# Optimization experiments

Measured on AMD Instinct MI355X. Metric: run time of the kernel, lower is better.

The kernel has to match this reference:

```python
import jax, jax.numpy as jnp
import numpy as np

def setup_inputs() -> dict:
    key = jax.random.key(0)
    ks = jax.random.split(key, 8)
    B, C, H, W = 4, 64, 64, 64
    Cr = C // 8
    s = 1.0 / np.sqrt(C)
    return {
        "x": jax.random.normal(ks[0], (B, C, H, W), jnp.float32),
        "wq": jax.random.normal(ks[1], (Cr, C), jnp.float32) * s,
        "bq": jax.random.normal(ks[2], (Cr,), jnp.float32) * 0.01,
        "wk": jax.random.normal(ks[3], (Cr, C), jnp.float32) * s,
        "bk": jax.random.normal(ks[4], (Cr,), jnp.float32) * 0.01,
        "wv": jax.random.normal(ks[5], (C, C), jnp.float32) * s,
        "bv": jax.random.normal(ks[6], (C,), jnp.float32) * 0.01,
        "gamma": jax.random.normal(ks[7], (1,), jnp.float32) * 0.1,
    }

def reference(x, wq, bq, wk, bk, wv, bv, gamma):
    B, C, H, W = x.shape
    N = H * W
    xf = x.reshape(B, C, N)  # 1x1 conv == pointwise linear over channel dim
    q = jnp.einsum("oc,bcn->bno", wq, xf) + bq[None, None, :]   # (B, N, Cr)
    k = jnp.einsum("oc,bcn->bon", wk, xf) + bk[None, :, None]   # (B, Cr, N)
    v = jnp.einsum("oc,bcn->bon", wv, xf) + bv[None, :, None]   # (B, C, N)
    attn = jnp.einsum("bno,bom->bnm", q, k)                     # (B, N, N)
    attn = jax.nn.softmax(attn, axis=-1)
    out = jnp.einsum("bcm,bnm->bcn", v, attn)                   # (B, C, N)
    out = out.reshape(B, C, H, W)
    return x + gamma[0] * out
```

## Files before the change

kernel.cpp:

```cpp
#include <hip/hip_runtime.h>

#define BB 4
#define CC 64
#define NN 4096

typedef __attribute__((ext_vector_type(8)))  short short8;
typedef __attribute__((ext_vector_type(4)))  short short4v;
typedef __attribute__((ext_vector_type(4)))  float f32x4;
typedef __attribute__((ext_vector_type(16))) float f32x16;
typedef unsigned short u16;

#define QWS_ELEMS (BB * NN * 8)

__device__ inline u16 f2bf(float x) {
    unsigned u = __float_as_uint(x);
    u = (u + 0x7fffu + ((u >> 16) & 1u)) >> 16;
    return (u16)u;
}
__device__ inline unsigned pack2rne(float a, float b) {
    return (unsigned)f2bf(a) | ((unsigned)f2bf(b) << 16);
}
__device__ inline unsigned permpack(float lo, float hi) {
    return __builtin_amdgcn_perm(__float_as_uint(hi), __float_as_uint(lo), 0x07060302);
}

__device__ inline void barrier_lgkm() {
    asm volatile("s_waitcnt lgkmcnt(0)\n\ts_barrier" ::: "memory");
}

union SH8 {
    short8 s;
    struct Halves { short4v lo, hi; } h;
    uint4 u;
};

__global__ __launch_bounds__(512) void proj_kernel(
    const float* __restrict__ x,
    const float* __restrict__ wq, const float* __restrict__ bq,
    const float* __restrict__ wk, const float* __restrict__ bk,
    const float* __restrict__ wv, const float* __restrict__ bv,
    u16* __restrict__ ws_u)
{
    u16* qws = ws_u;
    u16* kws = ws_u + QWS_ELEMS;
    u16* vws = ws_u + 2 * QWS_ELEMS;

    const int y   = blockIdx.y;
    const int pix = blockIdx.x * 512 + threadIdx.x;
    const int b   = pix >> 12;
    const int n   = pix & (NN - 1);
    const float* xb = x + ((size_t)b << 18) + n;

    if (y < 8) {
        const int v0 = y << 3;
        float av[8];
#pragma unroll
        for (int i = 0; i < 8; ++i) av[i] = bv[v0 + i];
#pragma unroll 8
        for (int c = 0; c < CC; ++c) {
            const float xv = xb[(size_t)c << 12];
#pragma unroll
            for (int i = 0; i < 8; ++i)
                av[i] += wv[(v0 + i) * CC + c] * xv;
        }
#pragma unroll
        for (int i = 0; i < 8; ++i)
            vws[(((size_t)((b << 6) + v0 + i)) << 12) + n] = f2bf(av[i]);
    } else {
        float aq[8], ak[8];
#pragma unroll
        for (int i = 0; i < 8; ++i) { aq[i] = bq[i]; ak[i] = bk[i]; }
#pragma unroll 8
        for (int c = 0; c < CC; ++c) {
            const float xv = xb[(size_t)c << 12];
#pragma unroll
            for (int i = 0; i < 8; ++i) {
                aq[i] += wq[i * CC + c] * xv;
                ak[i] += wk[i * CC + c] * xv;
            }
        }
        uint4 qp, kp;
        qp.x = pack2rne(aq[0], aq[1]); qp.y = pack2rne(aq[2], aq[3]);
        qp.z = pack2rne(aq[4], aq[5]); qp.w = pack2rne(aq[6], aq[7]);
        kp.x = pack2rne(ak[0], ak[1]); kp.y = pack2rne(ak[2], ak[3]);
        kp.z = pack2rne(ak[4], ak[5]); kp.w = pack2rne(ak[6], ak[7]);
        *(uint4*)&qws[(size_t)pix * 8] = qp;
        *(uint4*)&kws[(size_t)pix * 8] = kp;
    }
}

__global__ __launch_bounds__(512) void attn_kernel(
    const float* __restrict__ x, const float* __restrict__ gamma,
    const u16* __restrict__ ws_u, float* __restrict__ out)
{
    const u16* qws = ws_u;
    const u16* kws = ws_u + QWS_ELEMS;
    const u16* vws = ws_u + 2 * QWS_ELEMS;

    __shared__ __align__(16) char smem[34816 + 1024 + 256];
    u16*   v_t    = (u16*)smem;
    float* eb     = (float*)smem;
    float* l_part = (float*)(smem + 34816);
    float* l_inv  = (float*)(smem + 34816 + 1024);

    const int tid  = threadIdx.x;
    const int w    = tid >> 6;
    const int lane = tid & 63;
    const int l31  = lane & 31;
    const int lh   = lane >> 5;
    const int mh   = w >> 1;
    const int qh   = w & 1;

    const int b  = blockIdx.y;
    const int qb = blockIdx.x << 6;
    const int bN = b << 12;

    short8 qf = {0,0,0,0,0,0,0,0};
    short8 kf = {0,0,0,0,0,0,0,0};
    if (lane < 32) {
        qf = *(const short8*)(qws + (size_t)(bN + qb + (qh << 5) + l31) * 8);
        kf = *(const short8*)(kws + (size_t)(bN + (mh << 5) + l31) * 8);
    }
    short8 kn = kf;

    const int c_st = tid >> 3;
    const int o_st = (tid & 7) << 3;
    const u16* vgr = vws + (((size_t)((b << 6) + c_st)) << 12) + o_st;
    const int st0  = c_st * 132 + o_st;

    SH8 va0, va1, vb0, vb1;
    va0.s = *(const short8*)(vgr);
    va1.s = *(const short8*)(vgr + 64);
    *(short4v*)&v_t[st0]      = va0.h.lo;
    *(short4v*)&v_t[st0 + 4]  = va0.h.hi;
    *(short4v*)&v_t[st0 + 64] = va1.h.lo;
    *(short4v*)&v_t[st0 + 68] = va1.h.hi;
    va0.s = *(const short8*)(vgr + 128);
    va1.s = *(const short8*)(vgr + 192);

    const int rA = l31 * 132;
    const int rB = (32 + l31) * 132;
    const int mb = (mh << 5) + (lh << 2);

    f32x16 z16, acc0, acc1;
#pragma unroll
    for (int r = 0; r < 16; ++r) { z16[r] = 0.f; acc0[r] = 0.f; acc1[r] = 0.f; }
    float ls = 0.f;

    barrier_lgkm();

#pragma unroll 2
    for (int it = 0; it < 32; ++it) {
        const int buf = (it & 1) * (CC * 132);
        const int nxt = ((it + 1) & 31) << 7;
        const int nx2 = ((it + 2) & 31) << 7;

        vb0.s = *(const short8*)(vgr + nx2);
        vb1.s = *(const short8*)(vgr + nx2 + 64);
        if (lane < 32)
            kn = *(const short8*)(kws + (size_t)(bN + nxt + (mh << 5) + l31) * 8);

        f32x16 d = __builtin_amdgcn_mfma_f32_32x32x16_bf16(kf, qf, z16, 0, 0, 0);

        float p[16];
#pragma unroll
        for (int r = 0; r < 16; ++r) p[r] = __expf(d[r]);
        float s0 = 0.f, s1 = 0.f;
#pragma unroll
        for (int r = 0; r < 8; ++r) { s0 += p[2 * r]; s1 += p[2 * r + 1]; }
        ls += s0 + s1;

        SH8 A0, A1;
        A0.u.x = permpack(p[0],  p[1]);  A0.u.y = permpack(p[2],  p[3]);
        A0.u.z = permpack(p[4],  p[5]);  A0.u.w = permpack(p[6],  p[7]);
        A1.u.x = permpack(p[8],  p[9]);  A1.u.y = permpack(p[10], p[11]);
        A1.u.z = permpack(p[12], p[13]); A1.u.w = permpack(p[14], p[15]);

        SH8 B00, B01, B10, B11;
        B00.h.lo = *(const short4v*)&v_t[buf + rA + mb];
        B00.h.hi = *(const short4v*)&v_t[buf + rA + mb + 8];
        B01.h.lo = *(const short4v*)&v_t[buf + rB + mb];
        B01.h.hi = *(const short4v*)&v_t[buf + rB + mb + 8];
        B10.h.lo = *(const short4v*)&v_t[buf + rA + mb + 16];
        B10.h.hi = *(const short4v*)&v_t[buf + rA + mb + 24];
        B11.h.lo = *(const short4v*)&v_t[buf + rB + mb + 16];
        B11.h.hi = *(const short4v*)&v_t[buf + rB + mb + 24];

        acc0 = __builtin_amdgcn_mfma_f32_32x32x16_bf16(A0.s, B00.s, acc0, 0, 0, 0);
        acc1 = __builtin_amdgcn_mfma_f32_32x32x16_bf16(A0.s, B01.s, acc1, 0, 0, 0);
        acc0 = __builtin_amdgcn_mfma_f32_32x32x16_bf16(A1.s, B10.s, acc0, 0, 0, 0);
        acc1 = __builtin_amdgcn_mfma_f32_32x32x16_bf16(A1.s, B11.s, acc1, 0, 0, 0);

        const int ob = (CC * 132) - buf;
        *(short4v*)&v_t[ob + st0]      = va0.h.lo;
        *(short4v*)&v_t[ob + st0 + 4]  = va0.h.hi;
        *(short4v*)&v_t[ob + st0 + 64] = va1.h.lo;
        *(short4v*)&v_t[ob + st0 + 68] = va1.h.hi;
        va0 = vb0; va1 = vb1;
        kf = kn;

        barrier_lgkm();
    }

    float lt = ls + __shfl_xor(ls, 32, 64);
    if (lane < 32) l_part[(mh * 2 + qh) * 32 + l31] = lt;
    __syncthreads();
    if (w < 2 && lane < 32) {
        float s = l_part[(0 * 2 + qh) * 32 + l31] + l_part[(1 * 2 + qh) * 32 + l31]
                + l_part[(2 * 2 + qh) * 32 + l31] + l_part[(3 * 2 + qh) * 32 + l31];
        l_inv[qh * 32 + l31] = 1.0f / s;
    }

    if (mh >= 2) {
        float* e0 = &eb[(((mh - 2) << 2) + (qh << 1) + 0) * 1088 + lane * 17];
        float* e1 = &eb[(((mh - 2) << 2) + (qh << 1) + 1) * 1088 + lane * 17];
#pragma unroll
        for (int r = 0; r < 16; ++r) { e0[r] = acc0[r]; e1[r] = acc1[r]; }
    }
    __syncthreads();
    if (mh < 2) {
        const float* e0 = &eb[((mh << 2) + (qh << 1) + 0) * 1088 + lane * 17];
        const float* e1 = &eb[((mh << 2) + (qh << 1) + 1) * 1088 + lane * 17];
#pragma unroll
        for (int r = 0; r < 16; ++r) { acc0[r] += e0[r]; acc1[r] += e1[r]; }
    }
    __syncthreads();
    if (mh == 1) {
        float* e0 = &eb[((qh << 1) + 0) * 1088 + lane * 17];
        float* e1 = &eb[((qh << 1) + 1) * 1088 + lane * 17];
#pragma unroll
        for (int r = 0; r < 16; ++r) { e0[r] = acc0[r]; e1[r] = acc1[r]; }
    }
    __syncthreads();
    if (w < 2) {
        const float* e0 = &eb[((qh << 1) + 0) * 1088 + lane * 17];
        const float* e1 = &eb[((qh << 1) + 1) * 1088 + lane * 17];
#pragma unroll
        for (int r = 0; r < 16; ++r) { acc0[r] += e0[r]; acc1[r] += e1[r]; }

        f32x4 li[4];
#pragma unroll
        for (int k = 0; k < 4; ++k)
            li[k] = *(const f32x4*)&l_inv[qh * 32 + (k << 3) + (lh << 2)];
        const float g = gamma[0];
#pragma unroll
        for (int ch = 0; ch < 2; ++ch) {
            const int c = (ch << 5) + l31;
            const f32x16 a = ch ? acc1 : acc0;
            const size_t rowb = (((size_t)((b << 6) + c)) << 12) + qb + (qh << 5);
#pragma unroll
            for (int k = 0; k < 4; ++k) {
                const int q0 = (k << 3) + (lh << 2);
                const float4 xv = *(const float4*)&x[rowb + q0];
                float4 o;
                o.x = xv.x + g * a[4 * k + 0] * li[k][0];
                o.y = xv.y + g * a[4 * k + 1] * li[k][1];
                o.z = xv.z + g * a[4 * k + 2] * li[k][2];
                o.w = xv.w + g * a[4 * k + 3] * li[k][3];
                *(float4*)&out[rowb + q0] = o;
            }
        }
    }
}

extern "C" void kernel_launch(void* const* d_in, const int* in_sizes, int n_in,
                              void* d_out, int out_size, void* d_ws, size_t ws_size,
                              hipStream_t stream)
{
    const float* x     = (const float*)d_in[0];
    const float* wq    = (const float*)d_in[1];
    const float* bq    = (const float*)d_in[2];
    const float* wk    = (const float*)d_in[3];
    const float* bk    = (const float*)d_in[4];
    const float* wv    = (const float*)d_in[5];
    const float* bv    = (const float*)d_in[6];
    const float* gamma = (const float*)d_in[7];
    u16*   ws  = (u16*)d_ws;
    float* out = (float*)d_out;

    hipLaunchKernelGGL(proj_kernel, dim3(BB * NN / 512, 9), dim3(512), 0, stream,
                       x, wq, bq, wk, bk, wv, bv, ws);
    hipLaunchKernelGGL(attn_kernel, dim3(NN / 64, BB), dim3(512), 0, stream,
                       x, gamma, ws, out);
}
```

Baseline: 105.9 us.

## Shrink attention blocks to 32 queries and 4 waves, doubling grid size

Each attention block now handles 32 query rows with 4 waves that split the key dimension, instead of 64 query rows with 8 waves. The grid doubles to 512 blocks so the GPU's compute units have more blocks to schedule and balance. The V staging loads are reorganized so 256 threads fill the same 64x128 tile. The cost is that each block re-streams the full K and V for only half as many queries, doubling global and LDS traffic per unit of work. The 2x loop unroll is also dropped.

```diff
diff --git a/kernel.cpp b/kernel.cpp
--- a/kernel.cpp
+++ b/kernel.cpp
@@ -89,7 +89,7 @@
     }
 }
 
-__global__ __launch_bounds__(512) void attn_kernel(
+__global__ __launch_bounds__(256) void attn_kernel(
     const float* __restrict__ x, const float* __restrict__ gamma,
     const u16* __restrict__ ws_u, float* __restrict__ out)
 {
@@ -97,50 +97,49 @@
     const u16* kws = ws_u + QWS_ELEMS;
     const u16* vws = ws_u + 2 * QWS_ELEMS;
 
-    __shared__ __align__(16) char smem[34816 + 1024 + 256];
+    __shared__ __align__(16) char smem[33792 + 512 + 128];
     u16*   v_t    = (u16*)smem;
     float* eb     = (float*)smem;
-    float* l_part = (float*)(smem + 34816);
-    float* l_inv  = (float*)(smem + 34816 + 1024);
+    float* l_part = (float*)(smem + 33792);
+    float* l_inv  = (float*)(smem + 33792 + 512);
 
     const int tid  = threadIdx.x;
     const int w    = tid >> 6;
     const int lane = tid & 63;
     const int l31  = lane & 31;
     const int lh   = lane >> 5;
-    const int mh   = w >> 1;
-    const int qh   = w & 1;
 
     const int b  = blockIdx.y;
-    const int qb = blockIdx.x << 6;
+    const int qb = blockIdx.x << 5;
     const int bN = b << 12;
 
     short8 qf = {0,0,0,0,0,0,0,0};
     short8 kf = {0,0,0,0,0,0,0,0};
     if (lane < 32) {
-        qf = *(const short8*)(qws + (size_t)(bN + qb + (qh << 5) + l31) * 8);
-        kf = *(const short8*)(kws + (size_t)(bN + (mh << 5) + l31) * 8);
+        qf = *(const short8*)(qws + (size_t)(bN + qb + l31) * 8);
+        kf = *(const short8*)(kws + (size_t)(bN + (w << 5) + l31) * 8);
     }
     short8 kn = kf;
 
-    const int c_st = tid >> 3;
-    const int o_st = (tid & 7) << 3;
-    const u16* vgr = vws + (((size_t)((b << 6) + c_st)) << 12) + o_st;
-    const int st0  = c_st * 132 + o_st;
-
-    SH8 va0, va1, vb0, vb1;
-    va0.s = *(const short8*)(vgr);
-    va1.s = *(const short8*)(vgr + 64);
-    *(short4v*)&v_t[st0]      = va0.h.lo;
-    *(short4v*)&v_t[st0 + 4]  = va0.h.hi;
-    *(short4v*)&v_t[st0 + 64] = va1.h.lo;
-    *(short4v*)&v_t[st0 + 68] = va1.h.hi;
-    va0.s = *(const short8*)(vgr + 128);
-    va1.s = *(const short8*)(vgr + 192);
+    const int c_st = tid >> 2;
+    const int oq   = (tid & 3) << 3;
+    const u16* vgr = vws + (((size_t)((b << 6) + c_st)) << 12) + oq;
+    const int st0  = c_st * 132 + oq;
+
+    SH8 va[4], vb[4];
+#pragma unroll
+    for (int j = 0; j < 4; ++j) {
+        va[j].s = *(const short8*)(vgr + 32 * j);
+        *(short4v*)&v_t[st0 + 32 * j]     = va[j].h.lo;
+        *(short4v*)&v_t[st0 + 32 * j + 4] = va[j].h.hi;
+    }
+#pragma unroll
+    for (int j = 0; j < 4; ++j)
+        va[j].s = *(const short8*)(vgr + 128 + 32 * j);
 
     const int rA = l31 * 132;
     const int rB = (32 + l31) * 132;
-    const int mb = (mh << 5) + (lh << 2);
+    const int mb = (w << 5) + (lh << 2);
 
     f32x16 z16, acc0, acc1;
 #pragma unroll
@@ -149,16 +148,16 @@
 
     barrier_lgkm();
 
-#pragma unroll 2
     for (int it = 0; it < 32; ++it) {
-        const int buf = (it & 1) * (CC * 132);
+        const int buf = (it & 1) * 8448;
         const int nxt = ((it + 1) & 31) << 7;
         const int nx2 = ((it + 2) & 31) << 7;
 
-        vb0.s = *(const short8*)(vgr + nx2);
-        vb1.s = *(const short8*)(vgr + nx2 + 64);
+#pragma unroll
+        for (int j = 0; j < 4; ++j)
+            vb[j].s = *(const short8*)(vgr + nx2 + 32 * j);
         if (lane < 32)
-            kn = *(const short8*)(kws + (size_t)(bN + nxt + (mh << 5) + l31) * 8);
+            kn = *(const short8*)(kws + (size_t)(bN + nxt + (w << 5) + l31) * 8);
 
         f32x16 d = __builtin_amdgcn_mfma_f32_32x32x16_bf16(kf, qf, z16, 0, 0, 0);
 
@@ -191,63 +190,63 @@
         acc0 = __builtin_amdgcn_mfma_f32_32x32x16_bf16(A1.s, B10.s, acc0, 0, 0, 0);
         acc1 = __builtin_amdgcn_mfma_f32_32x32x16_bf16(A1.s, B11.s, acc1, 0, 0, 0);
 
-        const int ob = (CC * 132) - buf;
-        *(short4v*)&v_t[ob + st0]      = va0.h.lo;
-        *(short4v*)&v_t[ob + st0 + 4]  = va0.h.hi;
-        *(short4v*)&v_t[ob + st0 + 64] = va1.h.lo;
-        *(short4v*)&v_t[ob + st0 + 68] = va1.h.hi;
-        va0 = vb0; va1 = vb1;
+        const int ob = 8448 - buf;
+#pragma unroll
+        for (int j = 0; j < 4; ++j) {
+            *(short4v*)&v_t[ob + st0 + 32 * j]     = va[j].h.lo;
+            *(short4v*)&v_t[ob + st0 + 32 * j + 4] = va[j].h.hi;
+        }
+#pragma unroll
+        for (int j = 0; j < 4; ++j) va[j] = vb[j];
         kf = kn;
 
         barrier_lgkm();
     }
 
     float lt = ls + __shfl_xor(ls, 32, 64);
-    if (lane < 32) l_part[(mh * 2 + qh) * 32 + l31] = lt;
-    __syncthreads();
-    if (w < 2 && lane < 32) {
-        float s = l_part[(0 * 2 + qh) * 32 + l31] + l_part[(1 * 2 + qh) * 32 + l31]
-                + l_part[(2 * 2 + qh) * 32 + l31] + l_part[(3 * 2 + qh) * 32 + l31];
-        l_inv[qh * 32 + l31] = 1.0f / s;
-    }
-
-    if (mh >= 2) {
-        float* e0 = &eb[(((mh - 2) << 2) + (qh << 1) + 0) * 1088 + lane * 17];
-        float* e1 = &eb[(((mh - 2) << 2) + (qh << 1) + 1) * 1088 + lane * 17];
+    if (lane < 32) l_part[(w << 5) + l31] = lt;
+    __syncthreads();
+    if (w == 0 && lane < 32)
+        l_inv[l31] = 1.0f / (l_part[l31] + l_part[32 + l31] +
+                             l_part[64 + l31] + l_part[96 + l31]);
+
+    if (w >= 2) {
+        float* e0 = &eb[(((w - 2) << 1) + 0) * 1088 + lane * 17];
+        float* e1 = &eb[(((w - 2) << 1) + 1) * 1088 + lane * 17];
 #pragma unroll
         for (int r = 0; r < 16; ++r) { e0[r] = acc0[r]; e1[r] = acc1[r]; }
     }
     __syncthreads();
-    if (mh < 2) {
-        const float* e0 = &eb[((mh << 2) + (qh << 1) + 0) * 1088 + lane * 17];
-        const float* e1 = &eb[((mh << 2) + (qh << 1) + 1) * 1088 + lane * 17];
+    if (w < 2) {
+        const float* e0 = &eb[((w << 1) + 0) * 1088 + lane * 17];
+        const float* e1 = &eb[((w << 1) + 1) * 1088 + lane * 17];
 #pragma unroll
         for (int r = 0; r < 16; ++r) { acc0[r] += e0[r]; acc1[r] += e1[r]; }
     }
     __syncthreads();
-    if (mh == 1) {
-        float* e0 = &eb[((qh << 1) + 0) * 1088 + lane * 17];
-        float* e1 = &eb[((qh << 1) + 1) * 1088 + lane * 17];
+    if (w == 1) {
+        float* e0 = &eb[0 * 1088 + lane * 17];
+        float* e1 = &eb[1 * 1088 + lane * 17];
 #pragma unroll
         for (int r = 0; r < 16; ++r) { e0[r] = acc0[r]; e1[r] = acc1[r]; }
     }
     __syncthreads();
-    if (w < 2) {
-        const float* e0 = &eb[((qh << 1) + 0) * 1088 + lane * 17];
-        const float* e1 = &eb[((qh << 1) + 1) * 1088 + lane * 17];
+    if (w == 0) {
+        const float* e0 = &eb[0 * 1088 + lane * 17];
+        const float* e1 = &eb[1 * 1088 + lane * 17];
 #pragma unroll
         for (int r = 0; r < 16; ++r) { acc0[r] += e0[r]; acc1[r] += e1[r]; }
 
         f32x4 li[4];
 #pragma unroll
         for (int k = 0; k < 4; ++k)
-            li[k] = *(const f32x4*)&l_inv[qh * 32 + (k << 3) + (lh << 2)];
+            li[k] = *(const f32x4*)&l_inv[(k << 3) + (lh << 2)];
         const float g = gamma[0];
 #pragma unroll
         for (int ch = 0; ch < 2; ++ch) {
             const int c = (ch << 5) + l31;
             const f32x16 a = ch ? acc1 : acc0;
-            const size_t rowb = (((size_t)((b << 6) + c)) << 12) + qb + (qh << 5);
+            const size_t rowb = (((size_t)((b << 6) + c)) << 12) + qb;
 #pragma unroll
             for (int k = 0; k < 4; ++k) {
                 const int q0 = (k << 3) + (lh << 2);
@@ -280,6 +279,6 @@
 
     hipLaunchKernelGGL(proj_kernel, dim3(BB * NN / 512, 9), dim3(512), 0, stream,
                        x, wq, bq, wk, bk, wv, bv, ws);
-    hipLaunchKernelGGL(attn_kernel, dim3(NN / 64, BB), dim3(512), 0, stream,
+    hipLaunchKernelGGL(attn_kernel, dim3(NN / 32, BB), dim3(256), 0, stream,
                        x, gamma, ws, out);
 }
```

After: 111.5 us. 5.3% more time.

## Fuse projection and attention into one cooperative kernel with grid sync

Applied to the files above, without the earlier changes.

Merges the projection and attention kernels into a single cooperative launch of 256 blocks. A grid-wide sync separates the two phases. The projection phase is re-split so each block computes 10 output channels for 512 pixels. Q is pre-scaled by log2(e) so the softmax can use exp2f instead of __expf. This removes one kernel launch and its gap, at the cost of a grid barrier, scattered 2-byte q/k stores, and needing all 256 blocks to be co-resident.

```diff
diff --git a/kernel.cpp b/kernel.cpp
--- a/kernel.cpp
+++ b/kernel.cpp
@@ -1,8 +1,12 @@
 #include <hip/hip_runtime.h>
+#include <hip/hip_cooperative_groups.h>
+
+namespace cg = cooperative_groups;
 
 #define BB 4
 #define CC 64
 #define NN 4096
+#define LOG2E 1.44269504088896340736f
 
 typedef __attribute__((ext_vector_type(8)))  short short8;
 typedef __attribute__((ext_vector_type(4)))  short short4v;
@@ -17,9 +21,6 @@
     u = (u + 0x7fffu + ((u >> 16) & 1u)) >> 16;
     return (u16)u;
 }
-__device__ inline unsigned pack2rne(float a, float b) {
-    return (unsigned)f2bf(a) | ((unsigned)f2bf(b) << 16);
-}
 __device__ inline unsigned permpack(float lo, float hi) {
     return __builtin_amdgcn_perm(__float_as_uint(hi), __float_as_uint(lo), 0x07060302);
 }
@@ -34,68 +35,17 @@
     uint4 u;
 };
 
-__global__ __launch_bounds__(512) void proj_kernel(
+__global__ __launch_bounds__(512) void fused_kernel(
     const float* __restrict__ x,
     const float* __restrict__ wq, const float* __restrict__ bq,
     const float* __restrict__ wk, const float* __restrict__ bk,
     const float* __restrict__ wv, const float* __restrict__ bv,
-    u16* __restrict__ ws_u)
+    const float* __restrict__ gamma,
+    u16* __restrict__ ws_u, float* __restrict__ out)
 {
     u16* qws = ws_u;
     u16* kws = ws_u + QWS_ELEMS;
     u16* vws = ws_u + 2 * QWS_ELEMS;
-
-    const int y   = blockIdx.y;
-    const int pix = blockIdx.x * 512 + threadIdx.x;
-    const int b   = pix >> 12;
-    const int n   = pix & (NN - 1);
-    const float* xb = x + ((size_t)b << 18) + n;
-
-    if (y < 8) {
-        const int v0 = y << 3;
-        float av[8];
-#pragma unroll
-        for (int i = 0; i < 8; ++i) av[i] = bv[v0 + i];
-#pragma unroll 8
-        for (int c = 0; c < CC; ++c) {
-            const float xv = xb[(size_t)c << 12];
-#pragma unroll
-            for (int i = 0; i < 8; ++i)
-                av[i] += wv[(v0 + i) * CC + c] * xv;
-        }
-#pragma unroll
-        for (int i = 0; i < 8; ++i)
-            vws[(((size_t)((b << 6) + v0 + i)) << 12) + n] = f2bf(av[i]);
-    } else {
-        float aq[8], ak[8];
-#pragma unroll
-        for (int i = 0; i < 8; ++i) { aq[i] = bq[i]; ak[i] = bk[i]; }
-#pragma unroll 8
-        for (int c = 0; c < CC; ++c) {
-            const float xv = xb[(size_t)c << 12];
-#pragma unroll
-            for (int i = 0; i < 8; ++i) {
-                aq[i] += wq[i * CC + c] * xv;
-                ak[i] += wk[i * CC + c] * xv;
-            }
-        }
-        uint4 qp, kp;
-        qp.x = pack2rne(aq[0], aq[1]); qp.y = pack2rne(aq[2], aq[3]);
-        qp.z = pack2rne(aq[4], aq[5]); qp.w = pack2rne(aq[6], aq[7]);
-        kp.x = pack2rne(ak[0], ak[1]); kp.y = pack2rne(ak[2], ak[3]);
-        kp.z = pack2rne(ak[4], ak[5]); kp.w = pack2rne(ak[6], ak[7]);
-        *(uint4*)&qws[(size_t)pix * 8] = qp;
-        *(uint4*)&kws[(size_t)pix * 8] = kp;
-    }
-}
-
-__global__ __launch_bounds__(512) void attn_kernel(
-    const float* __restrict__ x, const float* __restrict__ gamma,
-    const u16* __restrict__ ws_u, float* __restrict__ out)
-{
-    const u16* qws = ws_u;
-    const u16* kws = ws_u + QWS_ELEMS;
-    const u16* vws = ws_u + 2 * QWS_ELEMS;
 
     __shared__ __align__(16) char smem[34816 + 1024 + 256];
     u16*   v_t    = (u16*)smem;
@@ -103,161 +53,205 @@
     float* l_part = (float*)(smem + 34816);
     float* l_inv  = (float*)(smem + 34816 + 1024);
 
-    const int tid  = threadIdx.x;
-    const int w    = tid >> 6;
-    const int lane = tid & 63;
-    const int l31  = lane & 31;
-    const int lh   = lane >> 5;
-    const int mh   = w >> 1;
-    const int qh   = w & 1;
-
-    const int b  = blockIdx.y;
-    const int qb = blockIdx.x << 6;
-    const int bN = b << 12;
-
-    short8 qf = {0,0,0,0,0,0,0,0};
-    short8 kf = {0,0,0,0,0,0,0,0};
-    if (lane < 32) {
-        qf = *(const short8*)(qws + (size_t)(bN + qb + (qh << 5) + l31) * 8);
-        kf = *(const short8*)(kws + (size_t)(bN + (mh << 5) + l31) * 8);
+    const int tid = threadIdx.x;
+    const int blk = blockIdx.x;
+
+    {
+        const int pg  = blk & 31;
+        const int sl  = blk >> 5;
+        const int o0  = sl * 10;
+        const int pix = (pg << 9) + tid;
+        const int b   = pix >> 12;
+        const int n   = pix & (NN - 1);
+        const float* xb = x + ((size_t)b << 18) + n;
+
+        const float* wrow[10];
+        float acc[10];
+#pragma unroll
+        for (int i = 0; i < 10; ++i) {
+            const int o = o0 + i;
+            if (o < 8)       { wrow[i] = wq + o * CC;        acc[i] = bq[o]; }
+            else if (o < 16) { wrow[i] = wk + (o - 8) * CC;  acc[i] = bk[o - 8]; }
+            else             { wrow[i] = wv + (o - 16) * CC; acc[i] = bv[o - 16]; }
+        }
+#pragma unroll 8
+        for (int c = 0; c < CC; ++c) {
+            const float xv = xb[(size_t)c << 12];
+#pragma unroll
+            for (int i = 0; i < 10; ++i)
+                acc[i] += wrow[i][c] * xv;
+        }
+#pragma unroll
+        for (int i = 0; i < 10; ++i) {
+            const int o = o0 + i;
+            if (o < 8)
+                qws[(size_t)pix * 8 + o] = f2bf(acc[i] * LOG2E);
+            else if (o < 16)
+                kws[(size_t)pix * 8 + (o - 8)] = f2bf(acc[i]);
+            else
+                vws[(((size_t)((b << 6) + (o - 16))) << 12) + n] = f2bf(acc[i]);
+        }
     }
-    short8 kn = kf;
-
-    const int c_st = tid >> 3;
-    const int o_st = (tid & 7) << 3;
-    const u16* vgr = vws + (((size_t)((b << 6) + c_st)) << 12) + o_st;
-    const int st0  = c_st * 132 + o_st;
-
-    SH8 va0, va1, vb0, vb1;
-    va0.s = *(const short8*)(vgr);
-    va1.s = *(const short8*)(vgr + 64);
-    *(short4v*)&v_t[st0]      = va0.h.lo;
-    *(short4v*)&v_t[st0 + 4]  = va0.h.hi;
-    *(short4v*)&v_t[st0 + 64] = va1.h.lo;
-    *(short4v*)&v_t[st0 + 68] = va1.h.hi;
-    va0.s = *(const short8*)(vgr + 128);
-    va1.s = *(const short8*)(vgr + 192);
-
-    const int rA = l31 * 132;
-    const int rB = (32 + l31) * 132;
-    const int mb = (mh << 5) + (lh << 2);
-
-    f32x16 z16, acc0, acc1;
-#pragma unroll
-    for (int r = 0; r < 16; ++r) { z16[r] = 0.f; acc0[r] = 0.f; acc1[r] = 0.f; }
-    float ls = 0.f;
-
-    barrier_lgkm();
+
+    __threadfence();
+    cg::this_grid().sync();
+
+    {
+        const int w    = tid >> 6;
+        const int lane = tid & 63;
+        const int l31  = lane & 31;
+        const int lh   = lane >> 5;
+        const int mh   = w >> 1;
+        const int qh   = w & 1;
+
+        const int b  = blk >> 6;
+        const int qb = (blk & 63) << 6;
+        const int bN = b << 12;
+
+        short8 qf = {0,0,0,0,0,0,0,0};
+        short8 kf = {0,0,0,0,0,0,0,0};
+        if (lane < 32) {
+            qf = *(const short8*)(qws + (size_t)(bN + qb + (qh << 5) + l31) * 8);
+            kf = *(const short8*)(kws + (size_t)(bN + (mh << 5) + l31) * 8);
+        }
+        short8 kn = kf;
+
+        const int c_st = tid >> 3;
+        const int o_st = (tid & 7) << 3;
+        const u16* vgr = vws + (((size_t)((b << 6) + c_st)) << 12) + o_st;
+        const int st0  = c_st * 132 + o_st;
+
+        SH8 va0, va1, vb0, vb1;
+        va0.s = *(const short8*)(vgr);
+        va1.s = *(const short8*)(vgr + 64);
+        *(short4v*)&v_t[st0]      = va0.h.lo;
+        *(short4v*)&v_t[st0 + 4]  = va0.h.hi;
+        *(short4v*)&v_t[st0 + 64] = va1.h.lo;
+        *(short4v*)&v_t[st0 + 68] = va1.h.hi;
+        va0.s = *(const short8*)(vgr + 128);
+        va1.s = *(const short8*)(vgr + 192);
+
+        const int rA = l31 * 132;
+        const int rB = (32 + l31) * 132;
+        const int mb = (mh << 5) + (lh << 2);
+
+        f32x16 z16, acc0, acc1;
+#pragma unroll
+        for (int r = 0; r < 16; ++r) { z16[r] = 0.f; acc0[r] = 0.f; acc1[r] = 0.f; }
+        float ls = 0.f;
+
+        barrier_lgkm();
 
 #pragma unroll 2
-    for (int it = 0; it < 32; ++it) {
-        const int buf = (it & 1) * (CC * 132);
-        const int nxt = ((it + 1) & 31) << 7;
-        const int nx2 = ((it + 2) & 31) << 7;
-
-        vb0.s = *(const short8*)(vgr + nx2);
-        vb1.s = *(const short8*)(vgr + nx2 + 64);
-        if (lane < 32)
-            kn = *(const short8*)(kws + (size_t)(bN + nxt + (mh << 5) + l31) * 8);
-
-        f32x16 d = __builtin_amdgcn_mfma_f32_32x32x16_bf16(kf, qf, z16, 0, 0, 0);
-
-        float p[16];
-#pragma unroll
-        for (int r = 0; r < 16; ++r) p[r] = __expf(d[r]);
-        float s0 = 0.f, s1 = 0.f;
-#pragma unroll
-        for (int r = 0; r < 8; ++r) { s0 += p[2 * r]; s1 += p[2 * r + 1]; }
-        ls += s0 + s1;
-
-        SH8 A0, A1;
-        A0.u.x = permpack(p[0],  p[1]);  A0.u.y = permpack(p[2],  p[3]);
-        A0.u.z = permpack(p[4],  p[5]);  A0.u.w = permpack(p[6],  p[7]);
-        A1.u.x = permpack(p[8],  p[9]);  A1.u.y = permpack(p[10], p[11]);
-        A1.u.z = permpack(p[12], p[13]); A1.u.w = permpack(p[14], p[15]);
-
-        SH8 B00, B01, B10, B11;
-        B00.h.lo = *(const short4v*)&v_t[buf + rA + mb];
-        B00.h.hi = *(const short4v*)&v_t[buf + rA + mb + 8];
-        B01.h.lo = *(const short4v*)&v_t[buf + rB + mb];
-        B01.h.hi = *(const short4v*)&v_t[buf + rB + mb + 8];
-        B10.h.lo = *(const short4v*)&v_t[buf + rA + mb + 16];
-        B10.h.hi = *(const short4v*)&v_t[buf + rA + mb + 24];
-        B11.h.lo = *(const short4v*)&v_t[buf + rB + mb + 16];
-        B11.h.hi = *(const short4v*)&v_t[buf + rB + mb + 24];
-
-        acc0 = __builtin_amdgcn_mfma_f32_32x32x16_bf16(A0.s, B00.s, acc0, 0, 0, 0);
-        acc1 = __builtin_amdgcn_mfma_f32_32x32x16_bf16(A0.s, B01.s, acc1, 0, 0, 0);
-        acc0 = __builtin_amdgcn_mfma_f32_32x32x16_bf16(A1.s, B10.s, acc0, 0, 0, 0);
-        acc1 = __builtin_amdgcn_mfma_f32_32x32x16_bf16(A1.s, B11.s, acc1, 0, 0, 0);
-
-        const int ob = (CC * 132) - buf;
-        *(short4v*)&v_t[ob + st0]      = va0.h.lo;
-        *(short4v*)&v_t[ob + st0 + 4]  = va0.h.hi;
-        *(short4v*)&v_t[ob + st0 + 64] = va1.h.lo;
-        *(short4v*)&v_t[ob + st0 + 68] = va1.h.hi;
-        va0 = vb0; va1 = vb1;
-        kf = kn;
-
-        barrier_lgkm();
-    }
-
-    float lt = ls + __shfl_xor(ls, 32, 64);
-    if (lane < 32) l_part[(mh * 2 + qh) * 32 + l31] = lt;
-    __syncthreads();
-    if (w < 2 && lane < 32) {
-        float s = l_part[(0 * 2 + qh) * 32 + l31] + l_part[(1 * 2 + qh) * 32 + l31]
-                + l_part[(2 * 2 + qh) * 32 + l31] + l_part[(3 * 2 + qh) * 32 + l31];
-        l_inv[qh * 32 + l31] = 1.0f / s;
-    }
-
-    if (mh >= 2) {
-        float* e0 = &eb[(((mh - 2) << 2) + (qh << 1) + 0) * 1088 + lane * 17];
-        float* e1 = &eb[(((mh - 2) << 2) + (qh << 1) + 1) * 1088 + lane * 17];
-#pragma unroll
-        for (int r = 0; r < 16; ++r) { e0[r] = acc0[r]; e1[r] = acc1[r]; }
-    }
-    __syncthreads();
-    if (mh < 2) {
-        const float* e0 = &eb[((mh << 2) + (qh << 1) + 0) * 1088 + lane * 17];
-        const float* e1 = &eb[((mh << 2) + (qh << 1) + 1) * 1088 + lane * 17];
-#pragma unroll
-        for (int r = 0; r < 16; ++r) { acc0[r] += e0[r]; acc1[r] += e1[r]; }
-    }
-    __syncthreads();
-    if (mh == 1) {
-        float* e0 = &eb[((qh << 1) + 0) * 1088 + lane * 17];
-        float* e1 = &eb[((qh << 1) + 1) * 1088 + lane * 17];
-#pragma unroll
-        for (int r = 0; r < 16; ++r) { e0[r] = acc0[r]; e1[r] = acc1[r]; }
-    }
-    __syncthreads();
-    if (w < 2) {
-        const float* e0 = &eb[((qh << 1) + 0) * 1088 + lane * 17];
-        const float* e1 = &eb[((qh << 1) + 1) * 1088 + lane * 17];
-#pragma unroll
-        for (int r = 0; r < 16; ++r) { acc0[r] += e0[r]; acc1[r] += e1[r]; }
-
-        f32x4 li[4];
-#pragma unroll
-        for (int k = 0; k < 4; ++k)
-            li[k] = *(const f32x4*)&l_inv[qh * 32 + (k << 3) + (lh << 2)];
-        const float g = gamma[0];
-#pragma unroll
-        for (int ch = 0; ch < 2; ++ch) {
-            const int c = (ch << 5) + l31;
-            const f32x16 a = ch ? acc1 : acc0;
-            const size_t rowb = (((size_t)((b << 6) + c)) << 12) + qb + (qh << 5);
-#pragma unroll
-            for (int k = 0; k < 4; ++k) {
-                const int q0 = (k << 3) + (lh << 2);
-                const float4 xv = *(const float4*)&x[rowb + q0];
-                float4 o;
-                o.x = xv.x + g * a[4 * k + 0] * li[k][0];
-                o.y = xv.y + g * a[4 * k + 1] * li[k][1];
-                o.z = xv.z + g * a[4 * k + 2] * li[k][2];
-                o.w = xv.w + g * a[4 * k + 3] * li[k][3];
-                *(float4*)&out[rowb + q0] = o;
+        for (int it = 0; it < 32; ++it) {
+            const int buf = (it & 1) * 8448;
+            const int nxt = ((it + 1) & 31) << 7;
+            const int nx2 = ((it + 2) & 31) << 7;
+
+            vb0.s = *(const short8*)(vgr + nx2);
+            vb1.s = *(const short8*)(vgr + nx2 + 64);
+            if (lane < 32)
+                kn = *(const short8*)(kws + (size_t)(bN + nxt + (mh << 5) + l31) * 8);
+
+            f32x16 d = __builtin_amdgcn_mfma_f32_32x32x16_bf16(kf, qf, z16, 0, 0, 0);
+
+            float p[16];
+#pragma unroll
+            for (int r = 0; r < 16; ++r) p[r] = exp2f(d[r]);
+            float s0 = 0.f, s1 = 0.f;
+#pragma unroll
+            for (int r = 0; r < 8; ++r) { s0 += p[2 * r]; s1 += p[2 * r + 1]; }
+            ls += s0 + s1;
+
+            SH8 A0, A1;
+            A0.u.x = permpack(p[0],  p[1]);  A0.u.y = permpack(p[2],  p[3]);
+            A0.u.z = permpack(p[4],  p[5]);  A0.u.w = permpack(p[6],  p[7]);
+            A1.u.x = permpack(p[8],  p[9]);  A1.u.y = permpack(p[10], p[11]);
+            A1.u.z = permpack(p[12], p[13]); A1.u.w = permpack(p[14], p[15]);
+
+            SH8 B00, B01, B10, B11;
+            B00.h.lo = *(const short4v*)&v_t[buf + rA + mb];
+            B00.h.hi = *(const short4v*)&v_t[buf + rA + mb + 8];
+            B01.h.lo = *(const short4v*)&v_t[buf + rB + mb];
+            B01.h.hi = *(const short4v*)&v_t[buf + rB + mb + 8];
+            B10.h.lo = *(const short4v*)&v_t[buf + rA + mb + 16];
+            B10.h.hi = *(const short4v*)&v_t[buf + rA + mb + 24];
+            B11.h.lo = *(const short4v*)&v_t[buf + rB + mb + 16];
+            B11.h.hi = *(const short4v*)&v_t[buf + rB + mb + 24];
+
+            acc0 = __builtin_amdgcn_mfma_f32_32x32x16_bf16(A0.s, B00.s, acc0, 0, 0, 0);
+            acc1 = __builtin_amdgcn_mfma_f32_32x32x16_bf16(A0.s, B01.s, acc1, 0, 0, 0);
+            acc0 = __builtin_amdgcn_mfma_f32_32x32x16_bf16(A1.s, B10.s, acc0, 0, 0, 0);
+            acc1 = __builtin_amdgcn_mfma_f32_32x32x16_bf16(A1.s, B11.s, acc1, 0, 0, 0);
+
+            const int ob = 8448 - buf;
+            *(short4v*)&v_t[ob + st0]      = va0.h.lo;
+            *(short4v*)&v_t[ob + st0 + 4]  = va0.h.hi;
+            *(short4v*)&v_t[ob + st0 + 64] = va1.h.lo;
+            *(short4v*)&v_t[ob + st0 + 68] = va1.h.hi;
+            va0 = vb0; va1 = vb1;
+            kf = kn;
+
+            barrier_lgkm();
+        }
+
+        float lt = ls + __shfl_xor(ls, 32, 64);
+        if (lane < 32) l_part[(mh * 2 + qh) * 32 + l31] = lt;
+        __syncthreads();
+        if (w < 2 && lane < 32) {
+            float s = l_part[(0 * 2 + qh) * 32 + l31] + l_part[(1 * 2 + qh) * 32 + l31]
+                    + l_part[(2 * 2 + qh) * 32 + l31] + l_part[(3 * 2 + qh) * 32 + l31];
+            l_inv[qh * 32 + l31] = 1.0f / s;
+        }
+
+        if (mh >= 2) {
+            float* e0 = &eb[(((mh - 2) << 2) + (qh << 1) + 0) * 1088 + lane * 17];
+            float* e1 = &eb[(((mh - 2) << 2) + (qh << 1) + 1) * 1088 + lane * 17];
+#pragma unroll
+            for (int r = 0; r < 16; ++r) { e0[r] = acc0[r]; e1[r] = acc1[r]; }
+        }
+        __syncthreads();
+        if (mh < 2) {
+            const float* e0 = &eb[((mh << 2) + (qh << 1) + 0) * 1088 + lane * 17];
+            const float* e1 = &eb[((mh << 2) + (qh << 1) + 1) * 1088 + lane * 17];
+#pragma unroll
+            for (int r = 0; r < 16; ++r) { acc0[r] += e0[r]; acc1[r] += e1[r]; }
+        }
+        __syncthreads();
+        if (mh == 1) {
+            float* e0 = &eb[((qh << 1) + 0) * 1088 + lane * 17];
+            float* e1 = &eb[((qh << 1) + 1) * 1088 + lane * 17];
+#pragma unroll
+            for (int r = 0; r < 16; ++r) { e0[r] = acc0[r]; e1[r] = acc1[r]; }
+        }
+        __syncthreads();
+        if (w < 2) {
+            const float* e0 = &eb[((qh << 1) + 0) * 1088 + lane * 17];
+            const float* e1 = &eb[((qh << 1) + 1) * 1088 + lane * 17];
+#pragma unroll
+            for (int r = 0; r < 16; ++r) { acc0[r] += e0[r]; acc1[r] += e1[r]; }
+
+            f32x4 li[4];
+#pragma unroll
+            for (int k = 0; k < 4; ++k)
+                li[k] = *(const f32x4*)&l_inv[qh * 32 + (k << 3) + (lh << 2)];
+            const float g = gamma[0];
+#pragma unroll
+            for (int ch = 0; ch < 2; ++ch) {
+                const int c = (ch << 5) + l31;
+                const f32x16 a = ch ? acc1 : acc0;
+                const size_t rowb = (((size_t)((b << 6) + c)) << 12) + qb + (qh << 5);
+#pragma unroll
+                for (int k = 0; k < 4; ++k) {
+                    const int q0 = (k << 3) + (lh << 2);
+                    const float4 xv = *(const float4*)&x[rowb + q0];
+                    float4 o;
+                    o.x = xv.x + g * a[4 * k + 0] * li[k][0];
+                    o.y = xv.y + g * a[4 * k + 1] * li[k][1];
+                    o.z = xv.z + g * a[4 * k + 2] * li[k][2];
+                    o.w = xv.w + g * a[4 * k + 3] * li[k][3];
+                    *(float4*)&out[rowb + q0] = o;
+                }
             }
         }
     }
@@ -278,8 +272,8 @@
     u16*   ws  = (u16*)d_ws;
     float* out = (float*)d_out;
 
-    hipLaunchKernelGGL(proj_kernel, dim3(BB * NN / 512, 9), dim3(512), 0, stream,
-                       x, wq, bq, wk, bk, wv, bv, ws);
-    hipLaunchKernelGGL(attn_kernel, dim3(NN / 64, BB), dim3(512), 0, stream,
-                       x, gamma, ws, out);
-}
+    void* args[] = {(void*)&x, (void*)&wq, (void*)&bq, (void*)&wk, (void*)&bk,
+                    (void*)&wv, (void*)&bv, (void*)&gamma, (void*)&ws, (void*)&out};
+    hipLaunchCooperativeKernel((void*)fused_kernel, dim3(256), dim3(512),
+                               args, 0, stream);
+}
```

After: 223.7 us. 2.11x slower.
